# Kernel tuning notes

Hardware: AMD Instinct MI355X
Metric: run time of the kernel (lower is better)

The kernel has to match this reference:

```python
import jax, jax.numpy as jnp
import numpy as np

T, N = 20, 192
D_EMB, D_H, D_REL = 32, 64, 32
D_TMP = D_REL + 2 * D_H  # 160 = rel_emb + h_self + h_neighbor


def setup_inputs() -> dict:
    key = jax.random.key(0)
    ks = jax.random.split(key, 16)
    g = lambda i, shape, s: jax.random.normal(ks[i], shape, jnp.float32) * s
    inp = {
        "nodes_abs": g(0, (T, N, 2), 1.0),
        "nodes_norm": g(1, (T, N, 2), 1.0),
        "shift_value": g(2, (T, N, 2), 1.0),
        # parameters (inputLayer, LSTMCell, 2 GCNs, outputLayer)
        "w_in": g(3, (D_EMB, 2), 0.2),
        "b_in": jnp.zeros((D_EMB,), jnp.float32),
        "w_ih": g(4, (4 * D_H, D_EMB), 0.1),
        "w_hh": g(5, (4 * D_H, D_H), 0.001),
        "b_ih": jnp.zeros((4 * D_H,), jnp.float32).at[D_H:2 * D_H].set(1.0),
        "b_hh": jnp.zeros((4 * D_H,), jnp.float32),
        "w_rel": g(6, (2, D_REL, 2), 0.1),
        "b_rel": jnp.zeros((2, D_REL), jnp.float32),
        "w_gate": g(7, (2, D_H, D_TMP), 0.1),
        "b_gate": jnp.zeros((2, D_H), jnp.float32),
        "w_ar": g(8, (2, D_TMP), 0.1),
        "b_ar": jnp.zeros((2,), jnp.float32),
        "w_nei": g(9, (2, D_H, D_H), 0.1),
        "w_out": g(10, (2, D_H), 0.1),
        "b_out": jnp.zeros((2,), jnp.float32),
        # int inputs
        "seq_list": jax.random.randint(ks[11], (T, N), 0, 2).astype(jnp.int32),
        "nei_list": jax.random.randint(ks[12], (T, N, N), 0, 2).astype(jnp.int32),
        "nei_num": jax.random.randint(ks[13], (T, N), 0, N).astype(jnp.int32),
    }
    return inp


def reference(nodes_abs, nodes_norm, shift_value, w_in, b_in, w_ih, w_hh, b_ih, b_hh,
              w_rel, b_rel, w_gate, b_gate, w_ar, b_ar, w_nei, w_out, b_out,
              seq_list, nei_list, nei_num):
    eps = 1e-6

    def gcn(p, corr, nei_f, h, c, o):
        # corr: (N,N,2) relative positions pos_i - pos_j; nei_f: (N,N) 0/1 mask
        r = jax.nn.relu(jnp.einsum('ijd,rd->ijr', corr, w_rel[p]) + b_rel[p])
        tmp = jnp.concatenate([r,
                               jnp.broadcast_to(h[:, None, :], (N, N, D_H)),
                               jnp.broadcast_to(h[None, :, :], (N, N, D_H))], axis=-1)
        gate = jax.nn.sigmoid(jnp.einsum('ijt,ht->ijh', tmp, w_gate[p]) + b_gate[p])
        score = jnp.einsum('ijt,t->ij', tmp, w_ar[p]) + b_ar[p]
        score = jnp.where(nei_f > 0, score, -1e9)
        pos = jax.nn.softmax(score, axis=1) * nei_f  # masked attention over neighbors j
        msg = jnp.einsum('ij,ijh,jh->ih', pos, gate, h)  # gated, attended aggregation
        c_new = c + msg @ w_nei[p].T
        h_new = o * jnp.tanh(c_new)
        v1 = jnp.sum(gate * nei_f[:, :, None]) / (jnp.sum(nei_f) * D_H + eps)
        v2 = jnp.sum(jnp.max(pos, axis=1)) / (jnp.sum(jnp.max(nei_f, axis=1)) + eps)
        v3 = jnp.sum(nei_f) / jnp.float32(N)
        return h_new, c_new, (v1, v2, v3)

    def step(carry, xs):
        h, c, v1s, v2s, v3s = carry
        abs_t, norm_t, seq_t, nei_t = xs
        m = seq_t > 0
        mf = m.astype(jnp.float32)
        nei_f = (nei_t > 0).astype(jnp.float32) * mf[:, None] * mf[None, :]
        corr = abs_t[:, None, :] - abs_t[None, :, :]  # corr_index[i,j] = pos_i - pos_j
        x = jax.nn.relu(norm_t @ w_in.T + b_in)  # dropout is identity in eval
        gates = x @ w_ih.T + b_ih + h @ w_hh.T + b_hh
        i_g, f_g, g_g, o_g = jnp.split(gates, 4, axis=-1)
        i_g = jax.nn.sigmoid(i_g); f_g = jax.nn.sigmoid(f_g); o_g = jax.nn.sigmoid(o_g)
        c1 = f_g * c + i_g * jnp.tanh(g_g)
        h1 = o_g * jnp.tanh(c1)
        h1, c1, look = gcn(0, corr, nei_f, h1, c1, o_g)
        h1, c1, _ = gcn(1, corr, nei_f, h1, c1, o_g)
        out_t = (h1 @ w_out.T + b_out) * mf[:, None]
        h = jnp.where(m[:, None], h1, h)  # only active nodes update state
        c = jnp.where(m[:, None], c1, c)
        return (h, c, v1s + look[0], v2s + look[1], v3s + look[2]), out_t

    h0 = jnp.zeros((N, D_H), jnp.float32)
    c0 = jnp.zeros((N, D_H), jnp.float32)
    z = jnp.float32(0.0)
    xs = (nodes_abs[:-1], nodes_norm[:-1], seq_list[:-1], nei_list[:-1])
    (h, c, v1, v2, v3), outs = jax.lax.scan(step, (h0, c0, z, z, z), xs)
    outputs = jnp.concatenate([outs, jnp.zeros((1, N, 2), jnp.float32)], axis=0)
    return outputs, h, c, (v1 / T, v2 / T, v3 / T)
```

## Files before the change

kernel.cpp:

```cpp
#include <hip/hip_runtime.h>
#include <hip/hip_bf16.h>

#define T_STEPS 20
#define NSTEP   19
#define NN      192
#define DH      64
#define DE      32

enum : int {
  O_H     = 0,
  O_C     = O_H   + NN*DH,
  O_HW0   = O_C   + NN*DH,
  O_HW1   = O_HW0 + NN*DH,
  O_CW    = O_HW1 + NN*DH,
  O_OG    = O_CW  + NN*DH,
  O_U1    = O_OG  + NN*DH,
  O_U20   = O_U1  + NN*DH,
  O_U21   = O_U20 + NN*DH,
  O_S1    = O_U21 + NN*DH,
  O_S20   = O_S1  + NN,
  O_S21   = O_S20 + NN,
  O_ACC   = O_S21 + NN,
  O_WIHT  = O_ACC + NSTEP*4 + 4,
  O_WHHT  = O_WIHT + 8192,
  O_BIH   = O_WHHT + 16384,
  O_WIN   = O_BIH  + 256,
  O_BIN   = O_WIN  + 64,
  O_WRELF = O_BIN  + 32,
  O_BRELF = O_WRELF+ 128,
  O_WGR   = O_BRELF+ 64,
  O_WGH1T = O_WGR  + 4096,
  O_WGH2T = O_WGH1T+ 8192,
  O_BGATE = O_WGH2T+ 8192,
  O_WARR  = O_BGATE+ 128,
  O_WARH1 = O_WARR + 64,
  O_WARH2 = O_WARH1+ 128,
  O_BAR   = O_WARH2+ 128,
  O_WNEIT = O_BAR  + 4,
  O_WOUT  = O_WNEIT+ 8192,
  O_BOUT  = O_WOUT + 128,
  O_TOTAL = O_BOUT + 2
};

typedef unsigned long long ull;

__device__ __forceinline__ float bf2f(__hip_bfloat16 v) { return __bfloat162float(v); }
__device__ __forceinline__ float sigm(float x) { return 1.0f / (1.0f + expf(-x)); }

__device__ __forceinline__ float ldf(const void* p, int idx, int isf32) {
  if (isf32) return ((const float*)p)[idx];
  return bf2f(((const __hip_bfloat16*)p)[idx]);
}
__device__ __forceinline__ void stf(void* p, int idx, float v, int isf32) {
  if (isf32) ((float*)p)[idx] = v;
  else       ((__hip_bfloat16*)p)[idx] = __float2bfloat16(v);
}

__device__ __forceinline__ int detect_f32(const void* wg, int wave, int lane, int* s_isf) {
  if (wave == 0) {
    const unsigned short* u = (const unsigned short*)wg;
    int bad = 0;
    for (int x = lane; x < 1024; x += 64) {
      float v = __uint_as_float(((unsigned)u[x]) << 16);
      if (!(fabsf(v) <= 4.0f)) bad++;
    }
    for (int o = 32; o >= 1; o >>= 1) bad += __shfl_xor(bad, o, 64);
    if (lane == 0) *s_isf = (bad > 64);
  }
  __syncthreads();
  return *s_isf;
}

__device__ __forceinline__ void lstm_prep_dev(
    float* __restrict__ F, const void* __restrict__ nnorm, int isf32,
    int t, int i, int tid, int wave, int lane, int load_hc,
    float* s_x, float* s_hc, float* s_cc, float* s_gates, float* s_h1)
{
  if (load_hc && wave == 0) { s_hc[lane] = F[O_H + i*DH + lane]; s_cc[lane] = F[O_C + i*DH + lane]; }
  if (wave == 1 && lane < DE) {
    float nx = ldf(nnorm, (t*NN + i)*2 + 0, isf32);
    float ny = ldf(nnorm, (t*NN + i)*2 + 1, isf32);
    s_x[lane] = fmaxf(nx*F[O_WIN + lane*2] + ny*F[O_WIN + lane*2 + 1] + F[O_BIN + lane], 0.f);
  }
  __syncthreads();
  {
    int G = tid;
    float acc = F[O_BIH + G];
    for (int e = 0; e < DE; e++) acc += F[O_WIHT + e*256 + G] * s_x[e];
    for (int k = 0; k < DH; k++) acc += F[O_WHHT + k*256 + G] * s_hc[k];
    s_gates[G] = acc;
  }
  __syncthreads();
  if (wave == 0) {
    float ig = sigm(s_gates[lane]);
    float fg = sigm(s_gates[64 + lane]);
    float gg = tanhf(s_gates[128 + lane]);
    float og = sigm(s_gates[192 + lane]);
    float c1 = fg * s_cc[lane] + ig * gg;
    float h1 = og * tanhf(c1);
    int idx = i*DH + lane;
    F[O_CW  + idx] = c1;
    F[O_HW0 + idx] = h1;
    F[O_OG  + idx] = og;
    s_h1[lane] = h1;
  }
  __syncthreads();
  {
    int idx = i*DH + lane;
    if (wave == 0) {
      float a = 0.f;
      const float* w = F + O_WGH1T + lane;
      for (int k = 0; k < DH; k++) a += w[k*DH] * s_h1[k];
      F[O_U1 + idx] = a;
    } else if (wave == 1) {
      float a = 0.f;
      const float* w = F + O_WGH2T + lane;
      for (int k = 0; k < DH; k++) a += w[k*DH] * s_h1[k];
      F[O_U20 + idx] = a;
    } else if (wave == 2) {
      float hp = s_h1[lane];
      float a1 = hp * F[O_WARH1 + lane];
      float a2 = hp * F[O_WARH2 + lane];
      for (int o = 32; o >= 1; o >>= 1) { a1 += __shfl_xor(a1, o, 64); a2 += __shfl_xor(a2, o, 64); }
      if (lane == 0) { F[O_S1 + i] = a1; F[O_S20 + i] = a2; }
    }
  }
}

__global__ __launch_bounds__(256) void k_init(float* __restrict__ F,
                       void* __restrict__ out,
                       const void* w_in,  const void* b_in,
                       const void* w_ih,  const void* w_hh,
                       const void* b_ih,  const void* b_hh,
                       const void* w_rel, const void* b_rel,
                       const void* w_gate,const void* b_gate,
                       const void* w_ar,  const void* b_ar,
                       const void* w_nei, const void* w_out,
                       const void* b_out) {
  __shared__ int s_isf;
  const int wave = threadIdx.x >> 6, lane = threadIdx.x & 63;
  const int isf32 = detect_f32(w_gate, wave, lane, &s_isf);
  int tid = blockIdx.x * blockDim.x + threadIdx.x;
  int stride = gridDim.x * blockDim.x;
  for (int x = tid; x < O_WIHT; x += stride) F[x] = 0.f;
  for (int x = tid; x < NN*2;  x += stride) stf(out, (T_STEPS-1)*NN*2 + x, 0.f, isf32);
  for (int x = tid; x < 8192;  x += stride) { int e = x >> 8, G = x & 255; F[O_WIHT + x] = ldf(w_ih, G*32 + e, isf32); }
  for (int x = tid; x < 16384; x += stride) { int k = x >> 8, G = x & 255; F[O_WHHT + x] = ldf(w_hh, G*64 + k, isf32); }
  for (int x = tid; x < 256;   x += stride) F[O_BIH + x] = ldf(b_ih, x, isf32) + ldf(b_hh, x, isf32);
  for (int x = tid; x < 64;    x += stride) F[O_WIN + x] = ldf(w_in, x, isf32);
  for (int x = tid; x < 32;    x += stride) F[O_BIN + x] = ldf(b_in, x, isf32);
  for (int x = tid; x < 128;   x += stride) F[O_WRELF + x] = ldf(w_rel, x, isf32);
  for (int x = tid; x < 64;    x += stride) F[O_BRELF + x] = ldf(b_rel, x, isf32);
  for (int x = tid; x < 4096;  x += stride) { int p = x >> 11, h = (x >> 5) & 63, d = x & 31;
    F[O_WGR + x] = ldf(w_gate, p*10240 + h*160 + d, isf32); }
  for (int x = tid; x < 8192;  x += stride) { int p = x >> 12, k = (x >> 6) & 63, h = x & 63;
    F[O_WGH1T + x] = ldf(w_gate, p*10240 + h*160 + 32 + k, isf32); }
  for (int x = tid; x < 8192;  x += stride) { int p = x >> 12, k = (x >> 6) & 63, h = x & 63;
    F[O_WGH2T + x] = ldf(w_gate, p*10240 + h*160 + 96 + k, isf32); }
  for (int x = tid; x < 128;   x += stride) F[O_BGATE + x] = ldf(b_gate, x, isf32);
  for (int x = tid; x < 64;    x += stride) { int p = x >> 5, d = x & 31; F[O_WARR + x] = ldf(w_ar, p*160 + d, isf32); }
  for (int x = tid; x < 128;   x += stride) { int p = x >> 6, k = x & 63; F[O_WARH1 + x] = ldf(w_ar, p*160 + 32 + k, isf32); }
  for (int x = tid; x < 128;   x += stride) { int p = x >> 6, k = x & 63; F[O_WARH2 + x] = ldf(w_ar, p*160 + 96 + k, isf32); }
  for (int x = tid; x < 2;     x += stride) F[O_BAR + x] = ldf(b_ar, x, isf32);
  for (int x = tid; x < 8192;  x += stride) { int p = x >> 12, k = (x >> 6) & 63, h = x & 63;
    F[O_WNEIT + x] = ldf(w_nei, p*4096 + h*64 + k, isf32); }
  for (int x = tid; x < 128;   x += stride) F[O_WOUT + x] = ldf(w_out, x, isf32);
  for (int x = tid; x < 2;     x += stride) F[O_BOUT + x] = ldf(b_out, x, isf32);
}

__global__ __launch_bounds__(256) void k_lstm0(float* __restrict__ F,
                                               const void* __restrict__ nnorm,
                                               const void* __restrict__ wg) {
  __shared__ float s_x[DE], s_hc[DH], s_cc[DH], s_gates[4*DH], s_h1[DH];
  __shared__ int s_isf;
  const int tid = threadIdx.x, wave = tid >> 6, lane = tid & 63;
  const int isf32 = detect_f32(wg, wave, lane, &s_isf);
  lstm_prep_dev(F, nnorm, isf32, 0, blockIdx.x, tid, wave, lane, 1,
                s_x, s_hc, s_cc, s_gates, s_h1);
}

__global__ __launch_bounds__(256) void k_gcn(float* __restrict__ F,
                                             const void* __restrict__ nabs,
                                             const void* __restrict__ nnorm,
                                             const int* __restrict__ seq,
                                             const int* __restrict__ nei,
                                             void* __restrict__ out,
                                             const void* __restrict__ wg,
                                             int t, int p, int last) {
  __shared__ float s_r[32*NN];
  __shared__ float s_score[NN], s_pos[NN], s_neif[NN];
  __shared__ int   s_jlist[NN];
  __shared__ float s_red[4*DH], s_v1[4], s_msg[DH], s_hprep[DH];
  __shared__ float s_x[DE], s_hc[DH], s_cc[DH], s_gates[4*DH], s_h1[DH];
  __shared__ int   s_isf, s_nv;

  const int tid = threadIdx.x, wave = tid >> 6, lane = tid & 63;
  const int i = blockIdx.x;
  const int isf32 = detect_f32(wg, wave, lane, &s_isf);
  const int m_i = seq[t*NN + i] > 0;
  const int HWr = p ? O_HW1 : O_HW0;
  const int U2r = p ? O_U21 : O_U20;
  const int S2r = p ? O_S21 : O_S20;

  if (wave < 3) {
    int j  = wave*64 + lane;
    int nf = m_i && (seq[t*NN + j] > 0) && (nei[(t*NN + i)*NN + j] > 0);
    s_neif[j] = nf ? 1.f : 0.f;
    float sc = 0.f;
    if (nf) {
      float cx = ldf(nabs, (t*NN + i)*2 + 0, isf32) - ldf(nabs, (t*NN + j)*2 + 0, isf32);
      float cy = ldf(nabs, (t*NN + i)*2 + 1, isf32) - ldf(nabs, (t*NN + j)*2 + 1, isf32);
      const float* wr = F + O_WRELF + p*64;
      const float* br = F + O_BRELF + p*32;
      const float* wa = F + O_WARR  + p*32;
      float dot = 0.f;
      for (int d = 0; d < 32; d++) {
        float rv = fmaxf(cx*wr[2*d] + cy*wr[2*d+1] + br[d], 0.f);
        s_r[d*NN + j] = rv;
        dot += rv * wa[d];
      }
      sc = dot + F[O_S1 + i] + F[S2r + j] + F[O_BAR + p];
    }
    s_score[j] = sc;
  }
  __syncthreads();

  if (wave == 0) {
    float n0 = s_neif[lane], n1 = s_neif[64+lane], n2 = s_neif[128+lane];
    float sc0 = s_score[lane], sc1 = s_score[64+lane], sc2 = s_score[128+lane];
    const float NEG = -3.0e38f;
    float mx = fmaxf(fmaxf(n0 > 0.f ? sc0 : NEG, n1 > 0.f ? sc1 : NEG),
                     n2 > 0.f ? sc2 : NEG);
    for (int o = 32; o >= 1; o >>= 1) mx = fmaxf(mx, __shfl_xor(mx, o, 64));
    float e0 = (n0 > 0.f) ? expf(sc0 - mx) : 0.f;
    float e1 = (n1 > 0.f) ? expf(sc1 - mx) : 0.f;
    float e2 = (n2 > 0.f) ? expf(sc2 - mx) : 0.f;
    float s = e0 + e1 + e2;
    for (int o = 32; o >= 1; o >>= 1) s += __shfl_xor(s, o, 64);
    float inv = (s > 0.f) ? 1.0f / s : 0.f;
    float p0 = e0*inv, p1 = e1*inv, p2 = e2*inv;
    s_pos[lane] = p0; s_pos[64+lane] = p1; s_pos[128+lane] = p2;
    ull m0 = __ballot(n0 > 0.f), m1 = __ballot(n1 > 0.f), m2 = __ballot(n2 > 0.f);
    ull lt = (1ull << lane) - 1ull;
    int c0 = __popcll(m0), c1 = __popcll(m1);
    if (n0 > 0.f) s_jlist[__popcll(m0 & lt)] = lane;
    if (n1 > 0.f) s_jlist[c0 + __popcll(m1 & lt)] = 64 + lane;
    if (n2 > 0.f) s_jlist[c0 + c1 + __popcll(m2 & lt)] = 128 + lane;
    if (lane == 0) s_nv = c0 + c1 + __popcll(m2);
    if (p == 0 && m_i) {
      float cnt = n0 + n1 + n2;
      float pm  = fmaxf(fmaxf(p0, p1), p2);
      for (int o = 32; o >= 1; o >>= 1) {
        cnt += __shfl_xor(cnt, o, 64);
        pm   = fmaxf(pm, __shfl_xor(pm, o, 64));
      }
      if (lane == 0 && cnt > 0.f) {
        atomicAdd(&F[O_ACC + t*4 + 1], cnt);
        atomicAdd(&F[O_ACC + t*4 + 2], pm);
        atomicAdd(&F[O_ACC + t*4 + 3], 1.f);
      }
    }
  }
  __syncthreads();

  {
    float msg = 0.f, v1 = 0.f;
    const int nv = s_nv;
    if (m_i && nv > 0) {
      float wreg[32];
      const float* wgp = F + O_WGR + p*2048 + lane*32;
#pragma unroll
      for (int d = 0; d < 32; d++) wreg[d] = wgp[d];
      float base = F[O_U1 + i*DH + lane] + F[O_BGATE + p*DH + lane];
      for (int k = wave; k < nv; k += 4) {
        int j = s_jlist[k];
        float u2 = F[U2r + j*DH + lane];
        float hw = F[HWr + j*DH + lane];
        float acc = base + u2;
#pragma unroll
        for (int d = 0; d < 32; d++) acc += s_r[d*NN + j] * wreg[d];
        float g = 1.0f / (1.0f + expf(-acc));
        v1 += g;
        msg += s_pos[j] * g * hw;
      }
    }
    s_red[wave*DH + lane] = msg;
    for (int o = 32; o >= 1; o >>= 1) v1 += __shfl_xor(v1, o, 64);
    if (lane == 0) s_v1[wave] = v1;
  }
  __syncthreads();

  if (wave == 0) {
    s_msg[lane] = s_red[lane] + s_red[64+lane] + s_red[128+lane] + s_red[192+lane];
    if (p == 0 && m_i && lane == 0) {
      float v1t = s_v1[0] + s_v1[1] + s_v1[2] + s_v1[3];
      atomicAdd(&F[O_ACC + t*4 + 0], v1t);
    }
  }
  __syncthreads();

  if (wave == 0) {
    int idx = i*DH + lane;
    float hcom, ccom = 0.f;
    if (m_i) {
      float cn = F[O_CW + idx];
      const float* wn = F + O_WNEIT + p*4096 + lane;
      for (int k = 0; k < DH; k++) cn += s_msg[k] * wn[k*DH];
      hcom = F[O_OG + idx] * tanhf(cn);
      F[O_CW + idx] = cn;
      ccom = cn;
      if (p == 1) { F[O_H + idx] = hcom; F[O_C + idx] = ccom; }
    } else {
      hcom = F[HWr + idx];
    }
    if (p == 0) F[O_HW1 + idx] = hcom;
    s_hprep[lane] = hcom;
    if (p == 1) {
      s_hc[lane] = m_i ? hcom : F[O_H + idx];
      s_cc[lane] = m_i ? ccom : F[O_C + idx];
    }
  }
  __syncthreads();

  if (p == 0) {
    int idx = i*DH + lane;
    if (wave == 0) {
      float a = 0.f;
      const float* w = F + O_WGH1T + 4096 + lane;
      for (int k = 0; k < DH; k++) a += w[k*DH] * s_hprep[k];
      F[O_U1 + idx] = a;
    } else if (wave == 1) {
      float a = 0.f;
      const float* w = F + O_WGH2T + 4096 + lane;
      for (int k = 0; k < DH; k++) a += w[k*DH] * s_hprep[k];
      F[O_U21 + idx] = a;
    } else if (wave == 2) {
      float hp = s_hprep[lane];
      float a1 = hp * F[O_WARH1 + DH + lane];
      float a2 = hp * F[O_WARH2 + DH + lane];
      for (int o = 32; o >= 1; o >>= 1) { a1 += __shfl_xor(a1, o, 64); a2 += __shfl_xor(a2, o, 64); }
      if (lane == 0) { F[O_S1 + i] = a1; F[O_S21 + i] = a2; }
    }
  } else {
    if (wave == 0 && lane < 2) {
      float a = 0.f;
      if (m_i) {
        a = F[O_BOUT + lane];
        const float* wo = F + O_WOUT + lane*DH;
        for (int h = 0; h < DH; h++) a += s_hprep[h] * wo[h];
      }
      stf(out, (t*NN + i)*2 + lane, a, isf32);
    }
    if (!last) {
      lstm_prep_dev(F, nnorm, isf32, t + 1, i, tid, wave, lane, 0,
                    s_x, s_hc, s_cc, s_gates, s_h1);
    } else {
      if (wave == 0) stf(out, T_STEPS*NN*2 + i*DH + lane,         s_hc[lane], isf32);
      if (wave == 1) stf(out, T_STEPS*NN*2 + NN*DH + i*DH + lane, s_cc[lane], isf32);
      if (i == 0 && tid == 0) {
        float v1 = 0.f, v2 = 0.f, v3 = 0.f;
        for (int tt = 0; tt < NSTEP; tt++) {
          float sg = F[O_ACC + tt*4 + 0], sn = F[O_ACC + tt*4 + 1];
          float sp = F[O_ACC + tt*4 + 2], sm = F[O_ACC + tt*4 + 3];
          v1 += sg / (sn * 64.f + 1e-6f);
          v2 += sp / (sm + 1e-6f);
          v3 += sn / 192.f;
        }
        int base = T_STEPS*NN*2 + 2*NN*DH;
        stf(out, base + 0, v1 / 20.f, isf32);
        stf(out, base + 1, v2 / 20.f, isf32);
        stf(out, base + 2, v3 / 20.f, isf32);
      }
    }
  }
}

extern "C" void kernel_launch(void* const* d_in, const int* in_sizes, int n_in,
                              void* d_out, int out_size, void* d_ws, size_t ws_size,
                              hipStream_t stream) {
  const void* nabs  = d_in[0];
  const void* nnorm = d_in[1];
  const int* seq = (const int*)d_in[18];
  const int* nei = (const int*)d_in[19];
  float* F = (float*)d_ws;

  k_init<<<NN, 256, 0, stream>>>(F, d_out,
      d_in[3], d_in[4], d_in[5], d_in[6], d_in[7], d_in[8], d_in[9], d_in[10],
      d_in[11], d_in[12], d_in[13], d_in[14], d_in[15], d_in[16], d_in[17]);
  k_lstm0<<<NN, 256, 0, stream>>>(F, nnorm, d_in[11]);
  for (int t = 0; t < NSTEP; t++) {
    k_gcn<<<NN, 256, 0, stream>>>(F, nabs, nnorm, seq, nei, d_out, d_in[11], t, 0, 0);
    k_gcn<<<NN, 256, 0, stream>>>(F, nabs, nnorm, seq, nei, d_out, d_in[11], t, 1, t == NSTEP - 1);
  }
}
```

Measured before the change: 657.1 us.

## Interleave U2/H buffers, transpose relation tile, cache dtype flag, use fast math

Several changes at once. The per-neighbour U2 and H values now sit interleaved so one float2 load fetches both. The relation-embedding shared tile is transposed to row-per-neighbour with padding. The next neighbour's data is prefetched in the gate loop. The dtype-detection scan now runs only once in the init kernel and is stored in the workspace. expf/tanhf are replaced with __expf-based fast versions. The aim is to cut global loads, LDS access cost and per-block detection overhead, at the cost of slightly lower transcendental accuracy.

```diff
diff --git a/kernel.cpp b/kernel.cpp
--- a/kernel.cpp
+++ b/kernel.cpp
@@ -9,19 +9,17 @@
 
 enum : int {
   O_H     = 0,
-  O_C     = O_H   + NN*DH,
-  O_HW0   = O_C   + NN*DH,
-  O_HW1   = O_HW0 + NN*DH,
-  O_CW    = O_HW1 + NN*DH,
-  O_OG    = O_CW  + NN*DH,
-  O_U1    = O_OG  + NN*DH,
-  O_U20   = O_U1  + NN*DH,
-  O_U21   = O_U20 + NN*DH,
-  O_S1    = O_U21 + NN*DH,
-  O_S20   = O_S1  + NN,
-  O_S21   = O_S20 + NN,
-  O_ACC   = O_S21 + NN,
-  O_WIHT  = O_ACC + NSTEP*4 + 4,
+  O_C     = O_H    + NN*DH,
+  O_UH0   = O_C    + NN*DH,
+  O_UH1   = O_UH0  + 2*NN*DH,
+  O_CW    = O_UH1  + 2*NN*DH,
+  O_OG    = O_CW   + NN*DH,
+  O_U1    = O_OG   + NN*DH,
+  O_S1    = O_U1   + NN*DH,
+  O_S20   = O_S1   + NN,
+  O_S21   = O_S20  + NN,
+  O_ACC   = O_S21  + NN,
+  O_WIHT  = O_ACC  + NSTEP*4 + 4,
   O_WHHT  = O_WIHT + 8192,
   O_BIH   = O_WHHT + 16384,
   O_WIN   = O_BIH  + 256,
@@ -39,13 +37,19 @@
   O_WNEIT = O_BAR  + 4,
   O_WOUT  = O_WNEIT+ 8192,
   O_BOUT  = O_WOUT + 128,
-  O_TOTAL = O_BOUT + 2
+  O_ISF   = O_BOUT + 2,
+  O_TOTAL = O_ISF  + 1
 };
 
 typedef unsigned long long ull;
 
 __device__ __forceinline__ float bf2f(__hip_bfloat16 v) { return __bfloat162float(v); }
-__device__ __forceinline__ float sigm(float x) { return 1.0f / (1.0f + expf(-x)); }
+__device__ __forceinline__ float sigm(float x) { return 1.0f / (1.0f + __expf(-x)); }
+__device__ __forceinline__ float tanh_fast(float x) {
+  float e = __expf(-2.0f * fabsf(x));
+  float r = (1.0f - e) / (1.0f + e);
+  return copysignf(r, x);
+}
 
 __device__ __forceinline__ float ldf(const void* p, int idx, int isf32) {
   if (isf32) return ((const float*)p)[idx];
@@ -56,17 +60,8 @@
   else       ((__hip_bfloat16*)p)[idx] = __float2bfloat16(v);
 }
 
-__device__ __forceinline__ int detect_f32(const void* wg, int wave, int lane, int* s_isf) {
-  if (wave == 0) {
-    const unsigned short* u = (const unsigned short*)wg;
-    int bad = 0;
-    for (int x = lane; x < 1024; x += 64) {
-      float v = __uint_as_float(((unsigned)u[x]) << 16);
-      if (!(fabsf(v) <= 4.0f)) bad++;
-    }
-    for (int o = 32; o >= 1; o >>= 1) bad += __shfl_xor(bad, o, 64);
-    if (lane == 0) *s_isf = (bad > 64);
-  }
+__device__ __forceinline__ int read_isf(const float* F, int tid, int* s_isf) {
+  if (tid == 0) *s_isf = (int)F[O_ISF];
   __syncthreads();
   return *s_isf;
 }
@@ -94,13 +89,13 @@
   if (wave == 0) {
     float ig = sigm(s_gates[lane]);
     float fg = sigm(s_gates[64 + lane]);
-    float gg = tanhf(s_gates[128 + lane]);
+    float gg = tanh_fast(s_gates[128 + lane]);
     float og = sigm(s_gates[192 + lane]);
     float c1 = fg * s_cc[lane] + ig * gg;
-    float h1 = og * tanhf(c1);
+    float h1 = og * tanh_fast(c1);
     int idx = i*DH + lane;
     F[O_CW  + idx] = c1;
-    F[O_HW0 + idx] = h1;
+    F[O_UH0 + 2*idx + 1] = h1;
     F[O_OG  + idx] = og;
     s_h1[lane] = h1;
   }
@@ -116,7 +111,7 @@
       float a = 0.f;
       const float* w = F + O_WGH2T + lane;
       for (int k = 0; k < DH; k++) a += w[k*DH] * s_h1[k];
-      F[O_U20 + idx] = a;
+      F[O_UH0 + 2*idx] = a;
     } else if (wave == 2) {
       float hp = s_h1[lane];
       float a1 = hp * F[O_WARH1 + lane];
@@ -139,7 +134,20 @@
                        const void* b_out) {
   __shared__ int s_isf;
   const int wave = threadIdx.x >> 6, lane = threadIdx.x & 63;
-  const int isf32 = detect_f32(w_gate, wave, lane, &s_isf);
+  if (wave == 0) {
+    const unsigned short* u = (const unsigned short*)w_gate;
+    int bad = 0;
+    for (int x = lane; x < 1024; x += 64) {
+      float v = __uint_as_float(((unsigned)u[x]) << 16);
+      if (!(fabsf(v) <= 4.0f)) bad++;
+    }
+    for (int o = 32; o >= 1; o >>= 1) bad += __shfl_xor(bad, o, 64);
+    if (lane == 0) s_isf = (bad > 64);
+  }
+  __syncthreads();
+  const int isf32 = s_isf;
+  if (blockIdx.x == 0 && threadIdx.x == 0) F[O_ISF] = (float)isf32;
+
   int tid = blockIdx.x * blockDim.x + threadIdx.x;
   int stride = gridDim.x * blockDim.x;
   for (int x = tid; x < O_WIHT; x += stride) F[x] = 0.f;
@@ -169,12 +177,11 @@
 }
 
 __global__ __launch_bounds__(256) void k_lstm0(float* __restrict__ F,
-                                               const void* __restrict__ nnorm,
-                                               const void* __restrict__ wg) {
+                                               const void* __restrict__ nnorm) {
   __shared__ float s_x[DE], s_hc[DH], s_cc[DH], s_gates[4*DH], s_h1[DH];
   __shared__ int s_isf;
   const int tid = threadIdx.x, wave = tid >> 6, lane = tid & 63;
-  const int isf32 = detect_f32(wg, wave, lane, &s_isf);
+  const int isf32 = read_isf(F, tid, &s_isf);
   lstm_prep_dev(F, nnorm, isf32, 0, blockIdx.x, tid, wave, lane, 1,
                 s_x, s_hc, s_cc, s_gates, s_h1);
 }
@@ -185,9 +192,8 @@
                                              const int* __restrict__ seq,
                                              const int* __restrict__ nei,
                                              void* __restrict__ out,
-                                             const void* __restrict__ wg,
                                              int t, int p, int last) {
-  __shared__ float s_r[32*NN];
+  __shared__ float s_rt[NN*33];
   __shared__ float s_score[NN], s_pos[NN], s_neif[NN];
   __shared__ int   s_jlist[NN];
   __shared__ float s_red[4*DH], s_v1[4], s_msg[DH], s_hprep[DH];
@@ -196,10 +202,9 @@
 
   const int tid = threadIdx.x, wave = tid >> 6, lane = tid & 63;
   const int i = blockIdx.x;
-  const int isf32 = detect_f32(wg, wave, lane, &s_isf);
+  const int isf32 = read_isf(F, tid, &s_isf);
   const int m_i = seq[t*NN + i] > 0;
-  const int HWr = p ? O_HW1 : O_HW0;
-  const int U2r = p ? O_U21 : O_U20;
+  const int UHr = p ? O_UH1 : O_UH0;
   const int S2r = p ? O_S21 : O_S20;
 
   if (wave < 3) {
@@ -216,7 +221,7 @@
       float dot = 0.f;
       for (int d = 0; d < 32; d++) {
         float rv = fmaxf(cx*wr[2*d] + cy*wr[2*d+1] + br[d], 0.f);
-        s_r[d*NN + j] = rv;
+        s_rt[j*33 + d] = rv;
         dot += rv * wa[d];
       }
       sc = dot + F[O_S1 + i] + F[S2r + j] + F[O_BAR + p];
@@ -232,9 +237,9 @@
     float mx = fmaxf(fmaxf(n0 > 0.f ? sc0 : NEG, n1 > 0.f ? sc1 : NEG),
                      n2 > 0.f ? sc2 : NEG);
     for (int o = 32; o >= 1; o >>= 1) mx = fmaxf(mx, __shfl_xor(mx, o, 64));
-    float e0 = (n0 > 0.f) ? expf(sc0 - mx) : 0.f;
-    float e1 = (n1 > 0.f) ? expf(sc1 - mx) : 0.f;
-    float e2 = (n2 > 0.f) ? expf(sc2 - mx) : 0.f;
+    float e0 = (n0 > 0.f) ? __expf(sc0 - mx) : 0.f;
+    float e1 = (n1 > 0.f) ? __expf(sc1 - mx) : 0.f;
+    float e2 = (n2 > 0.f) ? __expf(sc2 - mx) : 0.f;
     float s = e0 + e1 + e2;
     for (int o = 32; o >= 1; o >>= 1) s += __shfl_xor(s, o, 64);
     float inv = (s > 0.f) ? 1.0f / s : 0.f;
@@ -271,17 +276,23 @@
       const float* wgp = F + O_WGR + p*2048 + lane*32;
 #pragma unroll
       for (int d = 0; d < 32; d++) wreg[d] = wgp[d];
-      float base = F[O_U1 + i*DH + lane] + F[O_BGATE + p*DH + lane];
-      for (int k = wave; k < nv; k += 4) {
-        int j = s_jlist[k];
-        float u2 = F[U2r + j*DH + lane];
-        float hw = F[HWr + j*DH + lane];
-        float acc = base + u2;
+      float basev = F[O_U1 + i*DH + lane] + F[O_BGATE + p*DH + lane];
+      const float2* UH2 = (const float2*)(F + UHr);
+      int k = wave;
+      int jn = (k < nv) ? s_jlist[k] : 0;
+      float2 uhn = (k < nv) ? UH2[jn*DH + lane] : make_float2(0.f, 0.f);
+      for (; k < nv; k += 4) {
+        int j = jn;
+        float2 uh = uhn;
+        int kn = k + 4;
+        if (kn < nv) { jn = s_jlist[kn]; uhn = UH2[jn*DH + lane]; }
+        float acc = basev + uh.x;
+        const float* rr = &s_rt[j*33];
 #pragma unroll
-        for (int d = 0; d < 32; d++) acc += s_r[d*NN + j] * wreg[d];
-        float g = 1.0f / (1.0f + expf(-acc));
+        for (int d = 0; d < 32; d++) acc += rr[d] * wreg[d];
+        float g = sigm(acc);
         v1 += g;
-        msg += s_pos[j] * g * hw;
+        msg += s_pos[j] * g * uh.y;
       }
     }
     s_red[wave*DH + lane] = msg;
@@ -306,14 +317,14 @@
       float cn = F[O_CW + idx];
       const float* wn = F + O_WNEIT + p*4096 + lane;
       for (int k = 0; k < DH; k++) cn += s_msg[k] * wn[k*DH];
-      hcom = F[O_OG + idx] * tanhf(cn);
+      hcom = F[O_OG + idx] * tanh_fast(cn);
       F[O_CW + idx] = cn;
       ccom = cn;
       if (p == 1) { F[O_H + idx] = hcom; F[O_C + idx] = ccom; }
     } else {
-      hcom = F[HWr + idx];
-    }
-    if (p == 0) F[O_HW1 + idx] = hcom;
+      hcom = F[UHr + 2*idx + 1];
+    }
+    if (p == 0) F[O_UH1 + 2*idx + 1] = hcom;
     s_hprep[lane] = hcom;
     if (p == 1) {
       s_hc[lane] = m_i ? hcom : F[O_H + idx];
@@ -333,7 +344,7 @@
       float a = 0.f;
       const float* w = F + O_WGH2T + 4096 + lane;
       for (int k = 0; k < DH; k++) a += w[k*DH] * s_hprep[k];
-      F[O_U21 + idx] = a;
+      F[O_UH1 + 2*idx] = a;
     } else if (wave == 2) {
       float hp = s_hprep[lane];
       float a1 = hp * F[O_WARH1 + DH + lane];
@@ -387,9 +398,9 @@
   k_init<<<NN, 256, 0, stream>>>(F, d_out,
       d_in[3], d_in[4], d_in[5], d_in[6], d_in[7], d_in[8], d_in[9], d_in[10],
       d_in[11], d_in[12], d_in[13], d_in[14], d_in[15], d_in[16], d_in[17]);
-  k_lstm0<<<NN, 256, 0, stream>>>(F, nnorm, d_in[11]);
+  k_lstm0<<<NN, 256, 0, stream>>>(F, nnorm);
   for (int t = 0; t < NSTEP; t++) {
-    k_gcn<<<NN, 256, 0, stream>>>(F, nabs, nnorm, seq, nei, d_out, d_in[11], t, 0, 0);
-    k_gcn<<<NN, 256, 0, stream>>>(F, nabs, nnorm, seq, nei, d_out, d_in[11], t, 1, t == NSTEP - 1);
-  }
-}
+    k_gcn<<<NN, 256, 0, stream>>>(F, nabs, nnorm, seq, nei, d_out, t, 0, 0);
+    k_gcn<<<NN, 256, 0, stream>>>(F, nabs, nnorm, seq, nei, d_out, t, 1, t == NSTEP - 1);
+  }
+}
```

Result: no change. 648.3 us (-1.3%).
